# Kernel tuning notes

Hardware: AMD Instinct MI355X
Metric: run time of the kernel (lower is better)

The kernel has to match this reference:

```python
import jax, jax.numpy as jnp
import numpy as np

B, N, D = 2, 2048, 1024
H = 16
HD = D // H
SCALE = HD ** -0.5


def setup_inputs() -> dict:
    key = jax.random.key(0)
    k1, k2, kw, kb = jax.random.split(key, 4)
    x1 = jax.random.normal(k1, (B, N, D), dtype=jnp.float32)
    x2 = jax.random.normal(k2, (B, N, D), dtype=jnp.float32)
    # fused qkv linear: torch nn.Linear(dim, 3*dim): W [3D, D], b [3D]
    bound = 1.0 / np.sqrt(D)
    qkv_w = jax.random.uniform(kw, (3 * D, D), minval=-bound, maxval=bound, dtype=jnp.float32)
    qkv_b = jax.random.uniform(kb, (3 * D,), minval=-bound, maxval=bound, dtype=jnp.float32)
    return {"x1": x1, "x2": x2, "qkv_w": qkv_w, "qkv_b": qkv_b}


def reference(x1, x2, qkv_w, qkv_b):
    # qkv projections (only q from x1 and k,v from x2 are used by the module)
    q1 = (jnp.einsum('bnd,ed->bne', x1, qkv_w[:D]) + qkv_b[:D])
    k2 = (jnp.einsum('bnd,ed->bne', x2, qkv_w[D:2 * D]) + qkv_b[D:2 * D])
    v2 = (jnp.einsum('bnd,ed->bne', x2, qkv_w[2 * D:]) + qkv_b[2 * D:])
    # [B, H, N, HD]
    q1 = q1.reshape(B, N, H, HD).transpose(0, 2, 1, 3)
    k2 = k2.reshape(B, N, H, HD).transpose(0, 2, 1, 3)
    v2 = v2.reshape(B, N, H, HD).transpose(0, 2, 1, 3)
    # explicit QK^T -> softmax -> AV (materializes [B,H,N,N] like the original)
    scores = jnp.einsum('bhqd,bhkd->bhqk', q1, k2) * SCALE
    attn = jax.nn.softmax(scores, axis=-1)
    out = jnp.einsum('bhqk,bhkd->bhqd', attn, v2)
    # [B, N, D]; note original module skips out_proj (never applied in forward)
    return out.transpose(0, 2, 1, 3).reshape(B, N, D)
```

## Files before the change

kernel.cpp:

```cpp
#include <hip/hip_runtime.h>
#include <cstdint>
#include <cstddef>

#define B_   2
#define N_   2048
#define D_   1024
#define H_   16
#define HD_  64
#define QSCALE_ 0.18033688011112042f

typedef unsigned short u16;
typedef unsigned int   u32;
typedef __attribute__((ext_vector_type(8))) short short8;
typedef __attribute__((ext_vector_type(4))) float f32x4;
typedef __attribute__((ext_vector_type(4))) float fl4;
typedef __attribute__((ext_vector_type(4))) unsigned short us4;

#if __has_builtin(__builtin_amdgcn_exp2f)
#define EXP2F(x) __builtin_amdgcn_exp2f(x)
#else
#define EXP2F(x) exp2f(x)
#endif

__device__ __forceinline__ u16 f2bf(float f) {
  u32 u = __builtin_bit_cast(u32, f);
  u += 0x7fffu + ((u >> 16) & 1u);
  return (u16)(u >> 16);
}

__device__ __forceinline__ void gload16(const void* g, void* l) {
  typedef __attribute__((address_space(1))) unsigned int gu32;
  typedef __attribute__((address_space(3))) unsigned int lu32;
  __builtin_amdgcn_global_load_lds((gu32*)g, (lu32*)l, 16, 0, 0);
}

__global__ void convert_kernel(const fl4* __restrict__ x1, const fl4* __restrict__ x2,
                               const fl4* __restrict__ w,
                               us4* __restrict__ o1, us4* __restrict__ o2,
                               us4* __restrict__ ow) {
  const int NX = (B_ * N_ * D_) / 4;
  const int NW = (3 * D_ * D_) / 4;
  int stride = gridDim.x * blockDim.x;
  for (int i = blockIdx.x * blockDim.x + threadIdx.x; i < NX; i += stride) {
    fl4 a = x1[i];
    us4 r; r.x = f2bf(a.x); r.y = f2bf(a.y); r.z = f2bf(a.z); r.w = f2bf(a.w);
    o1[i] = r;
    fl4 b = x2[i];
    us4 s; s.x = f2bf(b.x); s.y = f2bf(b.y); s.z = f2bf(b.z); s.w = f2bf(b.w);
    o2[i] = s;
    if (i < NW) {
      fl4 c = w[i];
      us4 t; t.x = f2bf(c.x); t.y = f2bf(c.y); t.z = f2bf(c.z); t.w = f2bf(c.w);
      ow[i] = t;
    }
  }
}

__global__ __launch_bounds__(256) void qkv_gemm(
    const u16* __restrict__ x1b, const u16* __restrict__ x2b,
    const u16* __restrict__ wb, const float* __restrict__ bias,
    u16* __restrict__ Qb, u16* __restrict__ Kb, u16* __restrict__ Vtb) {
  const int z = blockIdx.z;
  const u16* X = (z == 0) ? x1b : x2b;
  const u16* W = wb + (size_t)z * D_ * D_;
  const float* bz = bias + z * D_;
  const int m0 = blockIdx.y * 128;
  const int e0 = blockIdx.x * 128;
  const int tid = threadIdx.x;
  const int lane = tid & 63;
  const int w = tid >> 6;
  const int wr = w >> 1, wc = w & 1;
  const int col = lane & 15, quad = lane >> 4;

  __shared__ __align__(16) u16 As[128 * 32];
  __shared__ __align__(16) u16 Bs[128 * 32];

  f32x4 acc[4][4] = {};

  int off0 = w * 2048 + lane * 16;
  int row0 = off0 >> 6;
  int ke0  = (off0 & 63) >> 1;
  int off1 = off0 + 1024;
  int row1 = off1 >> 6;
  int ke1  = (off1 & 63) >> 1;

  const u16* gA0 = X + (size_t)(m0 + row0) * D_ + ke0;
  const u16* gA1 = X + (size_t)(m0 + row1) * D_ + ke1;
  const u16* gB0 = W + (size_t)(e0 + row0) * D_ + ke0;
  const u16* gB1 = W + (size_t)(e0 + row1) * D_ + ke1;
  u16* lA0 = &As[w * 1024];
  u16* lA1 = &As[w * 1024 + 512];
  u16* lB0 = &Bs[w * 1024];
  u16* lB1 = &Bs[w * 1024 + 512];

  for (int k0 = 0; k0 < D_; k0 += 32) {
    __syncthreads();
    gload16(gA0 + k0, lA0);
    gload16(gA1 + k0, lA1);
    gload16(gB0 + k0, lB0);
    gload16(gB1 + k0, lB1);
    __syncthreads();

    short8 a[4], b[4];
#pragma unroll
    for (int i = 0; i < 4; ++i)
      a[i] = *(const short8*)&As[(wr * 64 + i * 16 + col) * 32 + quad * 8];
#pragma unroll
    for (int j = 0; j < 4; ++j)
      b[j] = *(const short8*)&Bs[(wc * 64 + j * 16 + col) * 32 + quad * 8];
#pragma unroll
    for (int i = 0; i < 4; ++i)
#pragma unroll
      for (int j = 0; j < 4; ++j)
        acc[i][j] = __builtin_amdgcn_mfma_f32_16x16x32_bf16(a[i], b[j], acc[i][j], 0, 0, 0);
  }

#pragma unroll
  for (int j = 0; j < 4; ++j) {
    int eg = e0 + wc * 64 + j * 16 + col;
    float bj = bz[eg];
    int h = eg >> 6, d = eg & 63;
#pragma unroll
    for (int i = 0; i < 4; ++i) {
#pragma unroll
      for (int r = 0; r < 4; ++r) {
        int m = m0 + wr * 64 + i * 16 + quad * 4 + r;
        int bb = m >> 11, n = m & (N_ - 1);
        float v = acc[i][j][r] + bj;
        if (z == 0) v *= QSCALE_;
        u16 o = f2bf(v);
        if (z == 0)      Qb [(((size_t)bb * H_ + h) * N_ + n) * HD_ + d] = o;
        else if (z == 1) Kb [(((size_t)bb * H_ + h) * N_ + n) * HD_ + d] = o;
        else             Vtb[(((size_t)bb * H_ + h) * HD_ + d) * N_ + n] = o;
      }
    }
  }
}

__global__ __launch_bounds__(256, 4) void attn_kernel(
    const u16* __restrict__ Qb, const u16* __restrict__ Kb,
    const u16* __restrict__ Vtb, float* __restrict__ out) {
  const int bh = blockIdx.y;
  const int bb = bh >> 4, h = bh & 15;
  const int q0 = blockIdx.x * 64;
  const int tid = threadIdx.x;
  const int lane = tid & 63;
  const int w = tid >> 6;
  const int col = lane & 15, quad = lane >> 4;

  const u16* __restrict__ Q  = Qb  + ((size_t)bh << 17);
  const u16* __restrict__ K  = Kb  + ((size_t)bh << 17);
  const u16* __restrict__ Vt = Vtb + ((size_t)bh << 17);

  __shared__ __align__(16) u16 Ks[2][64 * 64];
  __shared__ __align__(16) u16 Vs[2][64 * 64];
  __shared__ __align__(16) u16 P[4][16 * 64];
  u16* Pw = P[w];

  const int qrow = q0 + w * 16 + col;
  short8 qa0 = *(const short8*)&Q[qrow * HD_ + quad * 8];
  short8 qa1 = *(const short8*)&Q[qrow * HD_ + 32 + quad * 8];

  const int g0  = (quad ^ (col & 7)) * 8;
  const int g4  = g0 ^ 32;
  const int pg0 = (quad ^ ((col >> 1) & 7)) * 8;
  const int pg4 = pg0 ^ 32;
  const int c3 = col >> 3, c7 = col & 7;
  const int h2 = quad * 2;

  const int srow = tid >> 3;
  const int sg   = tid & 7;
  const int lw0 = srow * 64 + ((sg ^ (srow & 7)) * 8);
  const int lw1 = lw0 + 2048;
  const u16* gK = K + tid * 8;
  const u16* gV = Vt + srow * N_ + sg * 8;

  f32x4 accO[4] = {};
  float lsum[4] = {0.f, 0.f, 0.f, 0.f};

  short8 kA = *(const short8*)(gK);
  short8 kB = *(const short8*)(gK + 2048);
  short8 vA = *(const short8*)(gV);
  short8 vB = *(const short8*)(gV + 32 * N_);
  *(short8*)&Ks[0][lw0] = kA;
  *(short8*)&Ks[0][lw1] = kB;
  *(short8*)&Vs[0][lw0] = vA;
  *(short8*)&Vs[0][lw1] = vB;

  for (int t = 0; t < N_ / 64; ++t) {
    __syncthreads();
    const int cur = t & 1;
    if (t < N_ / 64 - 1) {
      const int k0n = (t + 1) * 64;
      kA = *(const short8*)(gK + k0n * 64);
      kB = *(const short8*)(gK + k0n * 64 + 2048);
      vA = *(const short8*)(gV + k0n);
      vB = *(const short8*)(gV + k0n + 32 * N_);
    }
    const u16* Kc = Ks[cur];
    const u16* Vc = Vs[cur];

    f32x4 s[4] = {};
    __builtin_amdgcn_s_setprio(1);
#pragma unroll
    for (int jn = 0; jn < 4; ++jn) {
      const int rb = (jn * 16 + col) * 64;
      short8 kb0 = *(const short8*)&Kc[rb + g0];
      short8 kb1 = *(const short8*)&Kc[rb + g4];
      s[jn] = __builtin_amdgcn_mfma_f32_16x16x32_bf16(qa0, kb0, s[jn], 0, 0, 0);
      s[jn] = __builtin_amdgcn_mfma_f32_16x16x32_bf16(qa1, kb1, s[jn], 0, 0, 0);
    }
    __builtin_amdgcn_s_setprio(0);

#pragma unroll
    for (int jn = 0; jn < 4; ++jn)
#pragma unroll
      for (int r = 0; r < 4; ++r) {
        float e = EXP2F(s[jn][r]);
        lsum[r] += e;
        Pw[(quad * 4 + r) * 64 + (((2 * jn + c3) ^ (h2 + (r >> 1))) * 8) + c7] =
            (u16)(__builtin_bit_cast(u32, e) >> 16);
      }
    __asm__ volatile("" ::: "memory");
    short8 pa0 = *(const short8*)&Pw[col * 64 + pg0];
    short8 pa1 = *(const short8*)&Pw[col * 64 + pg4];
    __asm__ volatile("" ::: "memory");

    __builtin_amdgcn_s_setprio(1);
#pragma unroll
    for (int jd = 0; jd < 4; ++jd) {
      const int rb = (jd * 16 + col) * 64;
      short8 vb0 = *(const short8*)&Vc[rb + g0];
      short8 vb1 = *(const short8*)&Vc[rb + g4];
      accO[jd] = __builtin_amdgcn_mfma_f32_16x16x32_bf16(pa0, vb0, accO[jd], 0, 0, 0);
      accO[jd] = __builtin_amdgcn_mfma_f32_16x16x32_bf16(pa1, vb1, accO[jd], 0, 0, 0);
    }
    __builtin_amdgcn_s_setprio(0);

    if (t < N_ / 64 - 1) {
      u16* Kn = (u16*)Ks[cur ^ 1];
      u16* Vn = (u16*)Vs[cur ^ 1];
      *(short8*)&Kn[lw0] = kA;
      *(short8*)&Kn[lw1] = kB;
      *(short8*)&Vn[lw0] = vA;
      *(short8*)&Vn[lw1] = vB;
    }
  }

#pragma unroll
  for (int r = 0; r < 4; ++r) {
    float v = lsum[r];
    v += __shfl_xor(v, 1);
    v += __shfl_xor(v, 2);
    v += __shfl_xor(v, 4);
    v += __shfl_xor(v, 8);
    lsum[r] = 1.0f / v;
  }

#pragma unroll
  for (int jd = 0; jd < 4; ++jd)
#pragma unroll
    for (int r = 0; r < 4; ++r) {
      int n = q0 + w * 16 + quad * 4 + r;
      int e = h * HD_ + jd * 16 + col;
      out[((size_t)bb * N_ + n) * D_ + e] = accO[jd][r] * lsum[r];
    }
}

extern "C" void kernel_launch(void* const* d_in, const int* in_sizes, int n_in,
                              void* d_out, int out_size, void* d_ws, size_t ws_size,
                              hipStream_t stream) {
  const float* x1 = (const float*)d_in[0];
  const float* x2 = (const float*)d_in[1];
  const float* qw = (const float*)d_in[2];
  const float* qb = (const float*)d_in[3];
  float* out = (float*)d_out;

  u16* ws   = (u16*)d_ws;
  u16* x1b  = ws;
  u16* x2b  = ws + 4194304;
  u16* wb   = ws + 8388608;
  u16* Qbf  = ws + 11534336;
  u16* Kbf  = ws + 15728640;
  u16* Vtb  = ws + 19922944;
  if (ws_size < (size_t)24117248 * 2) return;

  convert_kernel<<<dim3(1024), dim3(256), 0, stream>>>(
      (const fl4*)x1, (const fl4*)x2, (const fl4*)qw,
      (us4*)x1b, (us4*)x2b, (us4*)wb);

  qkv_gemm<<<dim3(8, 32, 3), dim3(256), 0, stream>>>(
      x1b, x2b, wb, qb, Qbf, Kbf, Vtb);

  attn_kernel<<<dim3(32, 32), dim3(256), 0, stream>>>(Qbf, Kbf, Vtb, out);
}
```

Baseline: 188.5 us.

## Switch attention to 32x32x16 MFMA with transposed scores and in-register P

Each wave now computes S^T for 32 query rows with 32x32x16 bf16 MFMA, so each block covers 128 queries and each K/V tile is reused across twice as many rows. The exponentiated scores are packed to bf16 with v_cvt_pk_bf16_f32 and rearranged with v_permlane32_swap to form the A operand of the PV MFMA directly. This removes the per-wave LDS round trip for P. The cost is a larger register footprint (launch bounds drop to 2 blocks per SM), half as many blocks in the grid, and a row-sum reduction through shared memory at the end.

```diff
diff --git a/kernel.cpp b/kernel.cpp
--- a/kernel.cpp
+++ b/kernel.cpp
@@ -13,8 +13,10 @@
 typedef unsigned int   u32;
 typedef __attribute__((ext_vector_type(8))) short short8;
 typedef __attribute__((ext_vector_type(4))) float f32x4;
+typedef __attribute__((ext_vector_type(16))) float f32x16;
 typedef __attribute__((ext_vector_type(4))) float fl4;
 typedef __attribute__((ext_vector_type(4))) unsigned short us4;
+typedef __attribute__((ext_vector_type(4))) unsigned int u32x4;
 
 #if __has_builtin(__builtin_amdgcn_exp2f)
 #define EXP2F(x) __builtin_amdgcn_exp2f(x)
@@ -26,6 +28,16 @@
   u32 u = __builtin_bit_cast(u32, f);
   u += 0x7fffu + ((u >> 16) & 1u);
   return (u16)(u >> 16);
+}
+
+__device__ __forceinline__ u32 cvtpk(float lo, float hi) {
+  u32 r;
+  asm("v_cvt_pk_bf16_f32 %0, %1, %2" : "=v"(r) : "v"(lo), "v"(hi));
+  return r;
+}
+
+__device__ __forceinline__ void plswap(u32& a, u32& b) {
+  asm volatile("v_permlane32_swap_b32 %0, %1" : "+v"(a), "+v"(b));
 }
 
 __device__ __forceinline__ void gload16(const void* g, void* l) {
@@ -137,16 +149,16 @@
   }
 }
 
-__global__ __launch_bounds__(256, 4) void attn_kernel(
+__global__ __launch_bounds__(256, 2) void attn_kernel(
     const u16* __restrict__ Qb, const u16* __restrict__ Kb,
     const u16* __restrict__ Vtb, float* __restrict__ out) {
   const int bh = blockIdx.y;
   const int bb = bh >> 4, h = bh & 15;
-  const int q0 = blockIdx.x * 64;
+  const int q0 = blockIdx.x * 128;
   const int tid = threadIdx.x;
   const int lane = tid & 63;
   const int w = tid >> 6;
-  const int col = lane & 15, quad = lane >> 4;
+  const int l31 = lane & 31, hf = lane >> 5, r7 = lane & 7;
 
   const u16* __restrict__ Q  = Qb  + ((size_t)bh << 17);
   const u16* __restrict__ K  = Kb  + ((size_t)bh << 17);
@@ -154,19 +166,13 @@
 
   __shared__ __align__(16) u16 Ks[2][64 * 64];
   __shared__ __align__(16) u16 Vs[2][64 * 64];
-  __shared__ __align__(16) u16 P[4][16 * 64];
-  u16* Pw = P[w];
-
-  const int qrow = q0 + w * 16 + col;
-  short8 qa0 = *(const short8*)&Q[qrow * HD_ + quad * 8];
-  short8 qa1 = *(const short8*)&Q[qrow * HD_ + 32 + quad * 8];
-
-  const int g0  = (quad ^ (col & 7)) * 8;
-  const int g4  = g0 ^ 32;
-  const int pg0 = (quad ^ ((col >> 1) & 7)) * 8;
-  const int pg4 = pg0 ^ 32;
-  const int c3 = col >> 3, c7 = col & 7;
-  const int h2 = quad * 2;
+  __shared__ float Ls[4][32];
+
+  const u16* Qr = Q + (size_t)(q0 + w * 32 + l31) * HD_;
+  short8 qf[4];
+#pragma unroll
+  for (int c = 0; c < 4; ++c)
+    qf[c] = *(const short8*)&Qr[c * 16 + hf * 8];
 
   const int srow = tid >> 3;
   const int sg   = tid & 7;
@@ -175,8 +181,8 @@
   const u16* gK = K + tid * 8;
   const u16* gV = Vt + srow * N_ + sg * 8;
 
-  f32x4 accO[4] = {};
-  float lsum[4] = {0.f, 0.f, 0.f, 0.f};
+  f32x16 accO[2] = {};
+  float lsum = 0.f;
 
   short8 kA = *(const short8*)(gK);
   short8 kB = *(const short8*)(gK + 2048);
@@ -200,40 +206,51 @@
     const u16* Kc = Ks[cur];
     const u16* Vc = Vs[cur];
 
-    f32x4 s[4] = {};
+    f32x16 sT[2] = {};
     __builtin_amdgcn_s_setprio(1);
 #pragma unroll
-    for (int jn = 0; jn < 4; ++jn) {
-      const int rb = (jn * 16 + col) * 64;
-      short8 kb0 = *(const short8*)&Kc[rb + g0];
-      short8 kb1 = *(const short8*)&Kc[rb + g4];
-      s[jn] = __builtin_amdgcn_mfma_f32_16x16x32_bf16(qa0, kb0, s[jn], 0, 0, 0);
-      s[jn] = __builtin_amdgcn_mfma_f32_16x16x32_bf16(qa1, kb1, s[jn], 0, 0, 0);
+    for (int kb = 0; kb < 2; ++kb) {
+      const int rb = (kb * 32 + l31) * 64;
+#pragma unroll
+      for (int c = 0; c < 4; ++c) {
+        short8 kf = *(const short8*)&Kc[rb + (((c * 2 + hf) ^ r7) * 8)];
+        sT[kb] = __builtin_amdgcn_mfma_f32_32x32x16_bf16(kf, qf[c], sT[kb], 0, 0, 0);
+      }
     }
     __builtin_amdgcn_s_setprio(0);
 
 #pragma unroll
-    for (int jn = 0; jn < 4; ++jn)
-#pragma unroll
-      for (int r = 0; r < 4; ++r) {
-        float e = EXP2F(s[jn][r]);
-        lsum[r] += e;
-        Pw[(quad * 4 + r) * 64 + (((2 * jn + c3) ^ (h2 + (r >> 1))) * 8) + c7] =
-            (u16)(__builtin_bit_cast(u32, e) >> 16);
+    for (int kb = 0; kb < 2; ++kb)
+#pragma unroll
+      for (int i = 0; i < 16; ++i) {
+        float e = EXP2F(sT[kb][i]);
+        lsum += e;
+        sT[kb][i] = e;
       }
-    __asm__ volatile("" ::: "memory");
-    short8 pa0 = *(const short8*)&Pw[col * 64 + pg0];
-    short8 pa1 = *(const short8*)&Pw[col * 64 + pg4];
-    __asm__ volatile("" ::: "memory");
+
+    short8 pf[4];
+#pragma unroll
+    for (int kc = 0; kc < 4; ++kc) {
+      const int kb = kc >> 1, o = (kc & 1) * 8;
+      u32 X = cvtpk(sT[kb][o + 0], sT[kb][o + 1]);
+      u32 Y = cvtpk(sT[kb][o + 4], sT[kb][o + 5]);
+      plswap(X, Y);
+      u32 Z = cvtpk(sT[kb][o + 2], sT[kb][o + 3]);
+      u32 W = cvtpk(sT[kb][o + 6], sT[kb][o + 7]);
+      plswap(Z, W);
+      u32x4 pw = {X, Z, Y, W};
+      pf[kc] = __builtin_bit_cast(short8, pw);
+    }
 
     __builtin_amdgcn_s_setprio(1);
 #pragma unroll
-    for (int jd = 0; jd < 4; ++jd) {
-      const int rb = (jd * 16 + col) * 64;
-      short8 vb0 = *(const short8*)&Vc[rb + g0];
-      short8 vb1 = *(const short8*)&Vc[rb + g4];
-      accO[jd] = __builtin_amdgcn_mfma_f32_16x16x32_bf16(pa0, vb0, accO[jd], 0, 0, 0);
-      accO[jd] = __builtin_amdgcn_mfma_f32_16x16x32_bf16(pa1, vb1, accO[jd], 0, 0, 0);
+    for (int db = 0; db < 2; ++db) {
+      const int rb = (db * 32 + l31) * 64;
+#pragma unroll
+      for (int kc = 0; kc < 4; ++kc) {
+        short8 vf = *(const short8*)&Vc[rb + (((kc * 2 + hf) ^ r7) * 8)];
+        accO[db] = __builtin_amdgcn_mfma_f32_32x32x16_bf16(pf[kc], vf, accO[db], 0, 0, 0);
+      }
     }
     __builtin_amdgcn_s_setprio(0);
 
@@ -247,23 +264,22 @@
     }
   }
 
-#pragma unroll
-  for (int r = 0; r < 4; ++r) {
-    float v = lsum[r];
-    v += __shfl_xor(v, 1);
-    v += __shfl_xor(v, 2);
-    v += __shfl_xor(v, 4);
-    v += __shfl_xor(v, 8);
-    lsum[r] = 1.0f / v;
-  }
-
-#pragma unroll
-  for (int jd = 0; jd < 4; ++jd)
-#pragma unroll
-    for (int r = 0; r < 4; ++r) {
-      int n = q0 + w * 16 + quad * 4 + r;
-      int e = h * HD_ + jd * 16 + col;
-      out[((size_t)bb * N_ + n) * D_ + e] = accO[jd][r] * lsum[r];
+  lsum += __shfl_xor(lsum, 32);
+  if (hf == 0) Ls[w][l31] = 1.0f / lsum;
+  __syncthreads();
+
+  float rinv[16];
+#pragma unroll
+  for (int r = 0; r < 16; ++r)
+    rinv[r] = Ls[w][(r & 3) + 8 * (r >> 2) + 4 * hf];
+
+#pragma unroll
+  for (int db = 0; db < 2; ++db)
+#pragma unroll
+    for (int r = 0; r < 16; ++r) {
+      int n = q0 + w * 32 + (r & 3) + 8 * (r >> 2) + 4 * hf;
+      int e = h * HD_ + db * 32 + l31;
+      out[((size_t)bb * N_ + n) * D_ + e] = accO[db][r] * rinv[r];
     }
 }
 
@@ -292,5 +308,5 @@
   qkv_gemm<<<dim3(8, 32, 3), dim3(256), 0, stream>>>(
       x1b, x2b, wb, qb, Qbf, Kbf, Vtb);
 
-  attn_kernel<<<dim3(32, 32), dim3(256), 0, stream>>>(Qbf, Kbf, Vtb, out);
-}
+  attn_kernel<<<dim3(16, 32), dim3(256), 0, stream>>>(Qbf, Kbf, Vtb, out);
+}
```

Result: faster. 172.1 us (-8.7%).
